# Optimization experiments

Measured on AMD Instinct MI355X. Metric: run time of the kernel, lower is better.

## Reference

```python
import jax, jax.numpy as jnp
import numpy as np

N_NODES = 50000
N_EDGES = 500000
IN_CH = 128
OUT_CH = 64
HEADS = 4


def setup_inputs() -> dict:
    key = jax.random.key(0)
    ks = jax.random.split(key, 9)
    x = jax.random.normal(ks[0], (N_NODES, IN_CH), dtype=jnp.float32)
    edge_index = jax.random.randint(ks[1], (2, N_EDGES), 0, N_NODES, dtype=jnp.int64)
    edge_weights = jax.random.uniform(ks[2], (N_EDGES, 1), dtype=jnp.float32)
    # xavier-uniform params, stored as [in, out] so y = x @ W
    def xavier(k, shape):
        fan_in, fan_out = shape
        lim = float(np.sqrt(6.0 / (fan_in + fan_out)))
        return jax.random.uniform(k, shape, minval=-lim, maxval=lim, dtype=jnp.float32)
    Wq = xavier(ks[3], (IN_CH, OUT_CH * HEADS))
    Wk = xavier(ks[4], (IN_CH, OUT_CH * HEADS))
    Wv = xavier(ks[5], (IN_CH, OUT_CH * HEADS))
    We = xavier(ks[6], (1, HEADS))
    Wout = xavier(ks[7], (OUT_CH * HEADS, OUT_CH))
    b_out = jnp.zeros((OUT_CH,), dtype=jnp.float32)
    return {"x": x, "edge_index": edge_index, "edge_weights": edge_weights,
            "Wq": Wq, "Wk": Wk, "Wv": Wv, "We": We, "Wout": Wout, "b_out": b_out}


def reference(x, edge_index, edge_weights, Wq, Wk, Wv, We, Wout, b_out):
    num_nodes = x.shape[0]
    src = edge_index[0]
    tgt = edge_index[1]
    x_src = x[src]                                    # [E, in]
    x_tgt = x[tgt]                                    # [E, in]
    q = (x_tgt @ Wq).reshape(-1, HEADS, OUT_CH)       # [E, H, C]
    k = (x_src @ Wk).reshape(-1, HEADS, OUT_CH)
    v = (x_src @ Wv).reshape(-1, HEADS, OUT_CH)
    attn = jnp.sum(q * k, axis=-1) / jnp.sqrt(jnp.float32(OUT_CH))  # [E, H]
    attn = attn + edge_weights @ We                   # [E, H]
    attn = jax.nn.leaky_relu(attn, negative_slope=0.2)
    attn = jax.nn.softmax(attn, axis=0)               # global softmax over edges (as in source)
    weighted_v = attn[..., None] * v                  # [E, H, C]
    out = jax.ops.segment_sum(weighted_v, tgt, num_segments=num_nodes)  # [N, H, C]
    out = out.reshape(num_nodes, HEADS * OUT_CH) @ Wout + b_out         # [N, out]
    if x.shape == out.shape:
        out = out + x
    return out
```

## Files before the change

kernel.cpp:

```cpp
#include <hip/hip_runtime.h>
#include <hip/hip_bf16.h>
#include <hip/hip_fp16.h>

#define N_NODES 50000
#define N_EDGES 500000
#define IN_CH   128
#define D       256
#define UDIM    512
#define OUT_CH  64
#define HEADS   4
#define NC      49
#define PCAP    1024

#define NB_X16  6250
#define NB_HIST 1954
#define NB_MB   256
#define NB_ZB   128
#define NB_GEMM 1564
#define NB_SCAT 1954

typedef _Float16 half8 __attribute__((ext_vector_type(8)));
typedef _Float16 half2_t __attribute__((ext_vector_type(2)));
typedef float   floatx4 __attribute__((ext_vector_type(4)));

__global__ __launch_bounds__(256) void k1_prep_kernel(const float* __restrict__ x,
                                                      __half* __restrict__ x16,
                                                      const int* __restrict__ ei,
                                                      int* __restrict__ cnt,
                                                      double* __restrict__ S,
                                                      const float* __restrict__ Wq,
                                                      const float* __restrict__ Wk,
                                                      const float* __restrict__ Wv,
                                                      const float* __restrict__ Wout,
                                                      __half* __restrict__ M16t,
                                                      __half* __restrict__ Zc16t) {
    __shared__ float sbuf[4][64];
    const int b = blockIdx.x, tid = threadIdx.x;
    if (b < NB_X16) {
        int i = b * 256 + tid;
        if (i < HEADS) S[i] = 0.0;
        int k = i * 4;
        if (k < N_NODES * IN_CH) {
            float4 v = *(const float4*)(x + k);
            union { __half2 h[2]; uint2 u; } pk;
            pk.h[0] = __floats2half2_rn(v.x, v.y);
            pk.h[1] = __floats2half2_rn(v.z, v.w);
            *(uint2*)(x16 + k) = pk.u;
        }
    } else if (b < NB_X16 + NB_HIST) {
        int e = (b - NB_X16) * 256 + tid;
        if (e < N_EDGES) atomicAdd(&cnt[ei[N_EDGES + e]], 1);
    } else if (b < NB_X16 + NB_HIST + NB_MB) {
        const int r = (b - NB_X16 - NB_HIST) * 2 + (tid >> 7);
        const int i = tid & 127;
        const int h = r >> 7, j = r & 127;
        float* buf = sbuf[tid >> 7];
        if (i < 64) buf[i] = Wk[(size_t)j * D + h * 64 + i];
        __syncthreads();
        const float4* qr = (const float4*)(Wq + (size_t)i * D + h * 64);
        float s = 0.f;
        #pragma unroll
        for (int c4 = 0; c4 < 16; ++c4) {
            float4 q = qr[c4];
            s += q.x * buf[c4 * 4] + q.y * buf[c4 * 4 + 1]
               + q.z * buf[c4 * 4 + 2] + q.w * buf[c4 * 4 + 3];
        }
        M16t[(size_t)r * IN_CH + i] = __float2half(s);
    } else {
        const int r = (b - NB_X16 - NB_HIST - NB_MB) * 4 + (tid >> 6);
        const int c = tid & 63;
        const int h = r >> 7, i = r & 127;
        float* buf = sbuf[tid >> 6];
        buf[c] = Wv[(size_t)i * D + h * 64 + c];
        __syncthreads();
        float s = 0.f;
        #pragma unroll 8
        for (int j = 0; j < 64; ++j)
            s += buf[j] * Wout[(size_t)(h * 64 + j) * OUT_CH + c];
        Zc16t[(size_t)c * UDIM + r] = __float2half(s);
    }
}

__global__ __launch_bounds__(256) void k2_scan_reduce_kernel(const int* __restrict__ cnt,
                                                             int* __restrict__ csum) {
    const int b = blockIdx.x, tid = threadIdx.x;
    const int lane = tid & 63, wid = tid >> 6;
    int s = 0;
    int idx0 = b * 1024 + tid * 4;
    #pragma unroll
    for (int i = 0; i < 4; ++i) {
        int idx = idx0 + i;
        if (idx < N_NODES) s += cnt[idx];
    }
    #pragma unroll
    for (int m = 1; m < 64; m <<= 1) s += __shfl_xor(s, m, 64);
    __shared__ int w4[4];
    if (lane == 0) w4[wid] = s;
    __syncthreads();
    if (tid == 0) csum[b] = w4[0] + w4[1] + w4[2] + w4[3];
}

__global__ __launch_bounds__(256) void k3_scan_chunks_kernel(int* __restrict__ cnt,
                                                             const int* __restrict__ csum,
                                                             int* __restrict__ rp) {
    __shared__ int stop[64];
    __shared__ int wsum[4];
    const int b = blockIdx.x, tid = threadIdx.x;
    const int lane = tid & 63, wid = tid >> 6;
    if (tid < 64) stop[tid] = (tid < NC) ? csum[tid] : 0;
    __syncthreads();
    int base = 0;
    for (int w = 0; w < b; ++w) base += stop[w];
    int v[4];
    const int idx0 = b * 1024 + tid * 4;
    #pragma unroll
    for (int i = 0; i < 4; ++i) {
        int idx = idx0 + i;
        v[i] = (idx < N_NODES) ? cnt[idx] : 0;
    }
    int tsum = v[0] + v[1] + v[2] + v[3];
    int x = tsum;
    #pragma unroll
    for (int d = 1; d < 64; d <<= 1) {
        int y = __shfl_up(x, d, 64);
        if (lane >= d) x += y;
    }
    if (lane == 63) wsum[wid] = x;
    __syncthreads();
    int woff = 0;
    for (int w = 0; w < wid; ++w) woff += wsum[w];
    int excl = base + woff + x - tsum;
    #pragma unroll
    for (int i = 0; i < 4; ++i) {
        int idx = idx0 + i;
        if (idx < N_NODES) { rp[idx] = excl; cnt[idx] = excl; }
        excl += v[i];
    }
}

__global__ __launch_bounds__(256) void k4_gemmu_scatter_kernel(const __half* __restrict__ x16,
                                                               const __half* __restrict__ M16t,
                                                               __half* __restrict__ u16,
                                                               const int* __restrict__ ei,
                                                               const float* __restrict__ ew,
                                                               int* __restrict__ cnt,
                                                               int2* __restrict__ payload) {
    __shared__ __half Ax[128][136];
    __shared__ __half Bm[128][136];
    const int tid = threadIdx.x;
    if (blockIdx.x >= NB_GEMM) {
        int e = (blockIdx.x - NB_GEMM) * 256 + tid;
        if (e < N_EDGES) {
            int s = ei[e], t = ei[N_EDGES + e];
            int pos = atomicAdd(&cnt[t], 1);
            payload[pos] = make_int2(s, __float_as_int(ew[e]));
        }
        return;
    }
    const int m0 = (blockIdx.x % 391) * 128;
    const int colbase = (blockIdx.x / 391) * 128;
    {
        const int r = tid >> 1, part = tid & 1;
        uint4 va[8];
        if (m0 + r < N_NODES) {
            const uint4* src = (const uint4*)(x16 + (size_t)(m0 + r) * IN_CH + part * 64);
            #pragma unroll
            for (int q = 0; q < 8; ++q) va[q] = src[q];
        } else {
            #pragma unroll
            for (int q = 0; q < 8; ++q) va[q] = make_uint4(0u, 0u, 0u, 0u);
        }
        uint4* da = (uint4*)&Ax[r][part * 64];
        #pragma unroll
        for (int q = 0; q < 8; ++q) da[q] = va[q];
        const uint4* sb = (const uint4*)(M16t + (size_t)(colbase + r) * IN_CH + part * 64);
        uint4* db = (uint4*)&Bm[r][part * 64];
        #pragma unroll
        for (int q = 0; q < 8; ++q) db[q] = sb[q];
    }
    __syncthreads();

    const int w = tid >> 6, lane = tid & 63;
    const int mrow = lane & 15, quad = lane >> 4;

    half8 a[2][4];
    #pragma unroll
    for (int mt = 0; mt < 2; ++mt)
        #pragma unroll
        for (int ks = 0; ks < 4; ++ks)
            a[mt][ks] = *(const half8*)&Ax[w * 32 + mt * 16 + mrow][ks * 32 + quad * 8];

    floatx4 acc[2][8];
    #pragma unroll
    for (int mt = 0; mt < 2; ++mt)
        #pragma unroll
        for (int nt = 0; nt < 8; ++nt)
            acc[mt][nt] = (floatx4){0.f, 0.f, 0.f, 0.f};

    #pragma unroll
    for (int nt = 0; nt < 8; ++nt) {
        #pragma unroll
        for (int ks = 0; ks < 4; ++ks) {
            half8 bfr = *(const half8*)&Bm[nt * 16 + mrow][ks * 32 + quad * 8];
            acc[0][nt] = __builtin_amdgcn_mfma_f32_16x16x32_f16(a[0][ks], bfr, acc[0][nt], 0, 0, 0);
            acc[1][nt] = __builtin_amdgcn_mfma_f32_16x16x32_f16(a[1][ks], bfr, acc[1][nt], 0, 0, 0);
        }
    }
    __syncthreads();
    #pragma unroll
    for (int mt = 0; mt < 2; ++mt)
        #pragma unroll
        for (int nt = 0; nt < 8; ++nt)
            #pragma unroll
            for (int r = 0; r < 4; ++r)
                Ax[w * 32 + mt * 16 + quad * 4 + r][nt * 16 + mrow] = __float2half(acc[mt][nt][r]);
    __syncthreads();
    {
        const int r = tid >> 1, part = tid & 1;
        if (m0 + r < N_NODES) {
            const uint4* s4 = (const uint4*)&Ax[r][part * 64];
            uint4* d4 = (uint4*)(u16 + (size_t)(m0 + r) * UDIM + colbase + part * 64);
            #pragma unroll
            for (int q = 0; q < 8; ++q) d4[q] = s4[q];
        }
    }
}

__global__ __launch_bounds__(256) void edge_fused_kernel(const __half* __restrict__ u16,
                                                         const __half* __restrict__ x16,
                                                         const int* __restrict__ rp,
                                                         const int* __restrict__ cnt,
                                                         const int2* __restrict__ payload,
                                                         const float* __restrict__ We,
                                                         __half* __restrict__ y16,
                                                         double* __restrict__ S) {
    __shared__ int2 pbuf[PCAP];
    __shared__ float sblk[4];
    const int tid = threadIdx.x;
    const int nodebase = blockIdx.x * 16;

    const int span0 = rp[nodebase];
    const int span1 = cnt[nodebase + 15];
    const int span_len = min(span1 - span0, PCAP);
    for (int i = tid; i < span_len; i += 256) pbuf[i] = payload[span0 + i];
    if (tid < 4) sblk[tid] = 0.f;
    __syncthreads();

    const int l16 = tid & 15;
    const int h = l16 >> 2;
    const int q = l16 & 3;
    const int node = nodebase + (tid >> 4);
    const float wev = We[h];

    uint4 ur4[4];
    {
        const uint4* ub = (const uint4*)(u16 + (size_t)node * UDIM + h * 128 + q * 32);
        ur4[0] = ub[0]; ur4[1] = ub[1]; ur4[2] = ub[2]; ur4[3] = ub[3];
    }
    const half2_t* uh = (const half2_t*)ur4;

    half2_t yacc[16];
    #pragma unroll
    for (int t = 0; t < 16; ++t) yacc[t] = (half2_t){(_Float16)0.f, (_Float16)0.f};

    float sacc = 0.f;
    const int start = rp[node];
    const int end = cnt[node];

    auto getpl = [&](int e) -> int2 {
        int idx = e - span0;
        return (idx < PCAP) ? pbuf[idx] : payload[e];
    };

    int2 pl = make_int2(0, 0);
    uint4 xr[4];
    if (start < end) {
        pl = getpl(start);
        const uint4* xb = (const uint4*)(x16 + (size_t)pl.x * IN_CH + q * 32);
        xr[0] = xb[0]; xr[1] = xb[1]; xr[2] = xb[2]; xr[3] = xb[3];
    }
    for (int e = start; e < end; ++e) {
        int2 pln = pl;
        uint4 xrn[4] = {xr[0], xr[1], xr[2], xr[3]};
        if (e + 1 < end) {
            pln = getpl(e + 1);
            const uint4* xb = (const uint4*)(x16 + (size_t)pln.x * IN_CH + q * 32);
            xrn[0] = xb[0]; xrn[1] = xb[1]; xrn[2] = xb[2]; xrn[3] = xb[3];
        }
        const half2_t* xh = (const half2_t*)xr;
        float dot = 0.f;
        #pragma unroll
        for (int t = 0; t < 16; ++t)
            dot = __builtin_amdgcn_fdot2(uh[t], xh[t], dot, false);
        dot += __shfl_xor(dot, 1, 16);
        dot += __shfl_xor(dot, 2, 16);
        float l = dot * 0.125f + __int_as_float(pl.y) * wev;
        l = fmaxf(l, 0.2f * l);
        float p = __expf(l);
        if (q == 0) sacc += p;
        half2_t p2 = (half2_t){(_Float16)p, (_Float16)p};
        #pragma unroll
        for (int t = 0; t < 16; ++t)
            yacc[t] = p2 * xh[t] + yacc[t];
        pl = pln;
        xr[0] = xrn[0]; xr[1] = xrn[1]; xr[2] = xrn[2]; xr[3] = xrn[3];
    }
    {
        uint4* yo = (uint4*)(y16 + (size_t)node * UDIM + h * 128 + q * 32);
        const uint4* ys = (const uint4*)yacc;
        yo[0] = ys[0]; yo[1] = ys[1]; yo[2] = ys[2]; yo[3] = ys[3];
    }
    __syncthreads();
    if (q == 0) atomicAdd(&sblk[h], sacc);
    __syncthreads();
    if (tid < 4) atomicAdd(&S[tid], (double)sblk[tid]);
}

__global__ __launch_bounds__(256) void gemm_out_mfma_kernel(const __half* __restrict__ y16,
                                                            const __half* __restrict__ Zc16t,
                                                            const double* __restrict__ S,
                                                            const float* __restrict__ b_out,
                                                            float* __restrict__ out) {
    __shared__ __half Ay[128][136];
    __shared__ __half Bz[64][136];
    __shared__ float invs_s[4];
    const int m0 = blockIdx.x * 128;
    const int tid = threadIdx.x;
    if (tid < 4) invs_s[tid] = (float)(1.0 / S[tid]);

    const int w = tid >> 6, lane = tid & 63;
    const int mrow = lane & 15, quad = lane >> 4;

    floatx4 result[2][4];
    #pragma unroll
    for (int mt = 0; mt < 2; ++mt)
        #pragma unroll
        for (int nt = 0; nt < 4; ++nt)
            result[mt][nt] = (floatx4){0.f, 0.f, 0.f, 0.f};

    for (int h = 0; h < HEADS; ++h) {
        {
            const int r = tid >> 1, part = tid & 1;
            uint4 va[8];
            if (m0 + r < N_NODES) {
                const uint4* src = (const uint4*)(y16 + (size_t)(m0 + r) * UDIM + h * 128 + part * 64);
                #pragma unroll
                for (int qq = 0; qq < 8; ++qq) va[qq] = src[qq];
            } else {
                #pragma unroll
                for (int qq = 0; qq < 8; ++qq) va[qq] = make_uint4(0u, 0u, 0u, 0u);
            }
            uint4* da = (uint4*)&Ay[r][part * 64];
            #pragma unroll
            for (int qq = 0; qq < 8; ++qq) da[qq] = va[qq];
        }
        {
            const int r = tid >> 2, part = tid & 3;
            const uint4* sb = (const uint4*)(Zc16t + (size_t)r * UDIM + h * 128 + part * 32);
            uint4* db = (uint4*)&Bz[r][part * 32];
            #pragma unroll
            for (int qq = 0; qq < 4; ++qq) db[qq] = sb[qq];
        }
        __syncthreads();

        half8 a[2][4];
        #pragma unroll
        for (int mt = 0; mt < 2; ++mt)
            #pragma unroll
            for (int ks = 0; ks < 4; ++ks)
                a[mt][ks] = *(const half8*)&Ay[w * 32 + mt * 16 + mrow][ks * 32 + quad * 8];

        floatx4 acc[2][4];
        #pragma unroll
        for (int mt = 0; mt < 2; ++mt)
            #pragma unroll
            for (int nt = 0; nt < 4; ++nt)
                acc[mt][nt] = (floatx4){0.f, 0.f, 0.f, 0.f};

        #pragma unroll
        for (int nt = 0; nt < 4; ++nt) {
            #pragma unroll
            for (int ks = 0; ks < 4; ++ks) {
                half8 bfr = *(const half8*)&Bz[nt * 16 + mrow][ks * 32 + quad * 8];
                acc[0][nt] = __builtin_amdgcn_mfma_f32_16x16x32_f16(a[0][ks], bfr, acc[0][nt], 0, 0, 0);
                acc[1][nt] = __builtin_amdgcn_mfma_f32_16x16x32_f16(a[1][ks], bfr, acc[1][nt], 0, 0, 0);
            }
        }
        const float inv = invs_s[h];
        #pragma unroll
        for (int mt = 0; mt < 2; ++mt)
            #pragma unroll
            for (int nt = 0; nt < 4; ++nt) {
                result[mt][nt][0] += inv * acc[mt][nt][0];
                result[mt][nt][1] += inv * acc[mt][nt][1];
                result[mt][nt][2] += inv * acc[mt][nt][2];
                result[mt][nt][3] += inv * acc[mt][nt][3];
            }
        __syncthreads();
    }
    float bcol[4];
    #pragma unroll
    for (int nt = 0; nt < 4; ++nt) bcol[nt] = b_out[nt * 16 + mrow];
    #pragma unroll
    for (int mt = 0; mt < 2; ++mt) {
        #pragma unroll
        for (int r = 0; r < 4; ++r) {
            int row = m0 + w * 32 + mt * 16 + quad * 4 + r;
            if (row < N_NODES) {
                float* dst = out + (size_t)row * OUT_CH;
                #pragma unroll
                for (int nt = 0; nt < 4; ++nt)
                    dst[nt * 16 + mrow] = result[mt][nt][r] + bcol[nt];
            }
        }
    }
}

extern "C" void kernel_launch(void* const* d_in, const int* in_sizes, int n_in,
                              void* d_out, int out_size, void* d_ws, size_t ws_size,
                              hipStream_t stream) {
    const float* x     = (const float*)d_in[0];
    const int*   ei    = (const int*)d_in[1];
    const float* ew    = (const float*)d_in[2];
    const float* Wq    = (const float*)d_in[3];
    const float* Wk    = (const float*)d_in[4];
    const float* Wv    = (const float*)d_in[5];
    const float* We    = (const float*)d_in[6];
    const float* Wout  = (const float*)d_in[7];
    const float* b_out = (const float*)d_in[8];
    float* out = (float*)d_out;

    __half* u16   = (__half*)d_ws;
    __half* y16   = u16 + (size_t)N_NODES * UDIM;
    __half* x16   = y16 + (size_t)N_NODES * UDIM;
    double* S     = (double*)(x16 + (size_t)N_NODES * IN_CH);
    __half* M16t  = (__half*)(S + HEADS);
    __half* Zc16t = M16t + UDIM * IN_CH;
    int*    rp    = (int*)(Zc16t + OUT_CH * UDIM);
    int*    cnt   = rp + N_NODES;
    int*    csum  = cnt + N_NODES;
    int2*   payload = (int2*)(csum + 64);

    hipMemsetAsync(cnt, 0, N_NODES * sizeof(int), stream);
    k1_prep_kernel<<<NB_X16 + NB_HIST + NB_MB + NB_ZB, 256, 0, stream>>>(
        x, x16, ei, cnt, S, Wq, Wk, Wv, Wout, M16t, Zc16t);
    k2_scan_reduce_kernel<<<NC, 256, 0, stream>>>(cnt, csum);
    k3_scan_chunks_kernel<<<NC, 256, 0, stream>>>(cnt, csum, rp);
    k4_gemmu_scatter_kernel<<<NB_GEMM + NB_SCAT, 256, 0, stream>>>(
        x16, M16t, u16, ei, ew, cnt, payload);
    edge_fused_kernel<<<N_NODES / 16, 256, 0, stream>>>(u16, x16, rp, cnt, payload, We, y16, S);
    gemm_out_mfma_kernel<<<(N_NODES + 127) / 128, 256, 0, stream>>>(y16, Zc16t, S, b_out, out);
}
```

Before: 270.5 us.

## Split GEMM/scatter kernel, drop LDS staging, double-buffer edge loop, use DPP reductions

The fused GEMM+scatter kernel is split into two separate launches. The u-projection GEMM now loads MFMA operands straight from global memory instead of staging them through LDS. The output GEMM is reworked the same way, with 64-row blocks and no shared memory. In the edge kernel, the per-edge loop gains a two-deep prefetch, splits the dot product into four independent accumulators, and replaces shfl_xor with DPP moves. These changes aim to cut LDS traffic, barriers and latency stalls, at the cost of redundant global/L2 loads and one extra kernel launch.

Result: slower. 310.8 us (+14.9%).

```diff
diff --git a/kernel.cpp b/kernel.cpp
--- a/kernel.cpp
+++ b/kernel.cpp
@@ -18,10 +18,18 @@
 #define NB_ZB   128
 #define NB_GEMM 1564
 #define NB_SCAT 1954
+#define NB_OUT  782
 
 typedef _Float16 half8 __attribute__((ext_vector_type(8)));
 typedef _Float16 half2_t __attribute__((ext_vector_type(2)));
 typedef float   floatx4 __attribute__((ext_vector_type(4)));
+
+__device__ __forceinline__ float dpp_xor1(float x) {
+    return __int_as_float(__builtin_amdgcn_mov_dpp(__float_as_int(x), 0xB1, 0xf, 0xf, true));
+}
+__device__ __forceinline__ float dpp_xor2(float x) {
+    return __int_as_float(__builtin_amdgcn_mov_dpp(__float_as_int(x), 0x4E, 0xf, 0xf, true));
+}
 
 __global__ __launch_bounds__(256) void k1_prep_kernel(const float* __restrict__ x,
                                                       __half* __restrict__ x16,
@@ -138,57 +146,25 @@
     }
 }
 
-__global__ __launch_bounds__(256) void k4_gemmu_scatter_kernel(const __half* __restrict__ x16,
-                                                               const __half* __restrict__ M16t,
-                                                               __half* __restrict__ u16,
-                                                               const int* __restrict__ ei,
-                                                               const float* __restrict__ ew,
-                                                               int* __restrict__ cnt,
-                                                               int2* __restrict__ payload) {
-    __shared__ __half Ax[128][136];
-    __shared__ __half Bm[128][136];
+__global__ __launch_bounds__(256) void k4a_gemm_kernel(const __half* __restrict__ x16,
+                                                       const __half* __restrict__ M16t,
+                                                       __half* __restrict__ u16) {
+    __shared__ __half Cst[128][136];
     const int tid = threadIdx.x;
-    if (blockIdx.x >= NB_GEMM) {
-        int e = (blockIdx.x - NB_GEMM) * 256 + tid;
-        if (e < N_EDGES) {
-            int s = ei[e], t = ei[N_EDGES + e];
-            int pos = atomicAdd(&cnt[t], 1);
-            payload[pos] = make_int2(s, __float_as_int(ew[e]));
-        }
-        return;
-    }
     const int m0 = (blockIdx.x % 391) * 128;
     const int colbase = (blockIdx.x / 391) * 128;
-    {
-        const int r = tid >> 1, part = tid & 1;
-        uint4 va[8];
-        if (m0 + r < N_NODES) {
-            const uint4* src = (const uint4*)(x16 + (size_t)(m0 + r) * IN_CH + part * 64);
-            #pragma unroll
-            for (int q = 0; q < 8; ++q) va[q] = src[q];
-        } else {
-            #pragma unroll
-            for (int q = 0; q < 8; ++q) va[q] = make_uint4(0u, 0u, 0u, 0u);
-        }
-        uint4* da = (uint4*)&Ax[r][part * 64];
-        #pragma unroll
-        for (int q = 0; q < 8; ++q) da[q] = va[q];
-        const uint4* sb = (const uint4*)(M16t + (size_t)(colbase + r) * IN_CH + part * 64);
-        uint4* db = (uint4*)&Bm[r][part * 64];
-        #pragma unroll
-        for (int q = 0; q < 8; ++q) db[q] = sb[q];
-    }
-    __syncthreads();
-
     const int w = tid >> 6, lane = tid & 63;
     const int mrow = lane & 15, quad = lane >> 4;
 
     half8 a[2][4];
     #pragma unroll
-    for (int mt = 0; mt < 2; ++mt)
-        #pragma unroll
-        for (int ks = 0; ks < 4; ++ks)
-            a[mt][ks] = *(const half8*)&Ax[w * 32 + mt * 16 + mrow][ks * 32 + quad * 8];
+    for (int mt = 0; mt < 2; ++mt) {
+        int row = m0 + w * 32 + mt * 16 + mrow;
+        row = min(row, N_NODES - 1);
+        const __half* ab = x16 + (size_t)row * IN_CH + quad * 8;
+        #pragma unroll
+        for (int ks = 0; ks < 4; ++ks) a[mt][ks] = *(const half8*)(ab + ks * 32);
+    }
 
     floatx4 acc[2][8];
     #pragma unroll
@@ -199,30 +175,43 @@
 
     #pragma unroll
     for (int nt = 0; nt < 8; ++nt) {
+        const __half* bb = M16t + (size_t)(colbase + nt * 16 + mrow) * IN_CH + quad * 8;
         #pragma unroll
         for (int ks = 0; ks < 4; ++ks) {
-            half8 bfr = *(const half8*)&Bm[nt * 16 + mrow][ks * 32 + quad * 8];
+            half8 bfr = *(const half8*)(bb + ks * 32);
             acc[0][nt] = __builtin_amdgcn_mfma_f32_16x16x32_f16(a[0][ks], bfr, acc[0][nt], 0, 0, 0);
             acc[1][nt] = __builtin_amdgcn_mfma_f32_16x16x32_f16(a[1][ks], bfr, acc[1][nt], 0, 0, 0);
         }
     }
-    __syncthreads();
+
     #pragma unroll
     for (int mt = 0; mt < 2; ++mt)
         #pragma unroll
         for (int nt = 0; nt < 8; ++nt)
             #pragma unroll
             for (int r = 0; r < 4; ++r)
-                Ax[w * 32 + mt * 16 + quad * 4 + r][nt * 16 + mrow] = __float2half(acc[mt][nt][r]);
+                Cst[w * 32 + mt * 16 + quad * 4 + r][nt * 16 + mrow] = __float2half(acc[mt][nt][r]);
     __syncthreads();
     {
         const int r = tid >> 1, part = tid & 1;
         if (m0 + r < N_NODES) {
-            const uint4* s4 = (const uint4*)&Ax[r][part * 64];
+            const uint4* s4 = (const uint4*)&Cst[r][part * 64];
             uint4* d4 = (uint4*)(u16 + (size_t)(m0 + r) * UDIM + colbase + part * 64);
             #pragma unroll
-            for (int q = 0; q < 8; ++q) d4[q] = s4[q];
-        }
+            for (int qq = 0; qq < 8; ++qq) d4[qq] = s4[qq];
+        }
+    }
+}
+
+__global__ __launch_bounds__(256) void k4b_scatter_kernel(const int* __restrict__ ei,
+                                                          const float* __restrict__ ew,
+                                                          int* __restrict__ cnt,
+                                                          int2* __restrict__ payload) {
+    int e = blockIdx.x * 256 + threadIdx.x;
+    if (e < N_EDGES) {
+        int s = ei[e], t = ei[N_EDGES + e];
+        int pos = atomicAdd(&cnt[t], 1);
+        payload[pos] = make_int2(s, __float_as_int(ew[e]));
     }
 }
 
@@ -271,40 +260,49 @@
         int idx = e - span0;
         return (idx < PCAP) ? pbuf[idx] : payload[e];
     };
-
-    int2 pl = make_int2(0, 0);
-    uint4 xr[4];
-    if (start < end) {
-        pl = getpl(start);
+    auto prefx = [&](const int2& pl, uint4* xr) {
         const uint4* xb = (const uint4*)(x16 + (size_t)pl.x * IN_CH + q * 32);
         xr[0] = xb[0]; xr[1] = xb[1]; xr[2] = xb[2]; xr[3] = xb[3];
-    }
-    for (int e = start; e < end; ++e) {
-        int2 pln = pl;
-        uint4 xrn[4] = {xr[0], xr[1], xr[2], xr[3]};
-        if (e + 1 < end) {
-            pln = getpl(e + 1);
-            const uint4* xb = (const uint4*)(x16 + (size_t)pln.x * IN_CH + q * 32);
-            xrn[0] = xb[0]; xrn[1] = xb[1]; xrn[2] = xb[2]; xrn[3] = xb[3];
-        }
+    };
+    auto process = [&](const int2& pl, const uint4* xr) {
         const half2_t* xh = (const half2_t*)xr;
-        float dot = 0.f;
-        #pragma unroll
-        for (int t = 0; t < 16; ++t)
-            dot = __builtin_amdgcn_fdot2(uh[t], xh[t], dot, false);
-        dot += __shfl_xor(dot, 1, 16);
-        dot += __shfl_xor(dot, 2, 16);
+        float d0 = 0.f, d1 = 0.f, d2 = 0.f, d3 = 0.f;
+        #pragma unroll
+        for (int t = 0; t < 4; ++t) {
+            d0 = __builtin_amdgcn_fdot2(uh[t],      xh[t],      d0, false);
+            d1 = __builtin_amdgcn_fdot2(uh[t + 4],  xh[t + 4],  d1, false);
+            d2 = __builtin_amdgcn_fdot2(uh[t + 8],  xh[t + 8],  d2, false);
+            d3 = __builtin_amdgcn_fdot2(uh[t + 12], xh[t + 12], d3, false);
+        }
+        float dot = (d0 + d1) + (d2 + d3);
+        dot += dpp_xor1(dot);
+        dot += dpp_xor2(dot);
         float l = dot * 0.125f + __int_as_float(pl.y) * wev;
         l = fmaxf(l, 0.2f * l);
         float p = __expf(l);
-        if (q == 0) sacc += p;
+        sacc += (q == 0) ? p : 0.f;
         half2_t p2 = (half2_t){(_Float16)p, (_Float16)p};
         #pragma unroll
         for (int t = 0; t < 16; ++t)
             yacc[t] = p2 * xh[t] + yacc[t];
-        pl = pln;
-        xr[0] = xrn[0]; xr[1] = xrn[1]; xr[2] = xrn[2]; xr[3] = xrn[3];
-    }
+    };
+
+    int2 plA = make_int2(0, 0), plB = make_int2(0, 0);
+    uint4 xrA[4], xrB[4];
+    if (start < end)     { plA = getpl(start);     prefx(plA, xrA); }
+    if (start + 1 < end) { plB = getpl(start + 1); prefx(plB, xrB); }
+
+    int e = start;
+    while (e < end) {
+        process(plA, xrA);
+        if (e + 2 < end) { plA = getpl(e + 2); prefx(plA, xrA); }
+        ++e;
+        if (e >= end) break;
+        process(plB, xrB);
+        if (e + 2 < end) { plB = getpl(e + 2); prefx(plB, xrB); }
+        ++e;
+    }
+
     {
         uint4* yo = (uint4*)(y16 + (size_t)node * UDIM + h * 128 + q * 32);
         const uint4* ys = (const uint4*)yacc;
@@ -321,97 +319,54 @@
                                                             const double* __restrict__ S,
                                                             const float* __restrict__ b_out,
                                                             float* __restrict__ out) {
-    __shared__ __half Ay[128][136];
-    __shared__ __half Bz[64][136];
-    __shared__ float invs_s[4];
-    const int m0 = blockIdx.x * 128;
     const int tid = threadIdx.x;
-    if (tid < 4) invs_s[tid] = (float)(1.0 / S[tid]);
-
     const int w = tid >> 6, lane = tid & 63;
     const int mrow = lane & 15, quad = lane >> 4;
-
-    floatx4 result[2][4];
-    #pragma unroll
-    for (int mt = 0; mt < 2; ++mt)
-        #pragma unroll
-        for (int nt = 0; nt < 4; ++nt)
-            result[mt][nt] = (floatx4){0.f, 0.f, 0.f, 0.f};
+    const int row0 = blockIdx.x * 64 + w * 16;
+
+    float invs[4];
+    #pragma unroll
+    for (int hh = 0; hh < HEADS; ++hh) invs[hh] = (float)(1.0 / S[hh]);
+
+    floatx4 result[4];
+    #pragma unroll
+    for (int nt = 0; nt < 4; ++nt) result[nt] = (floatx4){0.f, 0.f, 0.f, 0.f};
 
     for (int h = 0; h < HEADS; ++h) {
+        half8 a[4];
         {
-            const int r = tid >> 1, part = tid & 1;
-            uint4 va[8];
-            if (m0 + r < N_NODES) {
-                const uint4* src = (const uint4*)(y16 + (size_t)(m0 + r) * UDIM + h * 128 + part * 64);
-                #pragma unroll
-                for (int qq = 0; qq < 8; ++qq) va[qq] = src[qq];
-            } else {
-                #pragma unroll
-                for (int qq = 0; qq < 8; ++qq) va[qq] = make_uint4(0u, 0u, 0u, 0u);
+            int arow = min(row0 + mrow, N_NODES - 1);
+            const __half* ab = y16 + (size_t)arow * UDIM + h * 128 + quad * 8;
+            #pragma unroll
+            for (int ks = 0; ks < 4; ++ks) a[ks] = *(const half8*)(ab + ks * 32);
+        }
+        const float inv = invs[h];
+        #pragma unroll
+        for (int nt = 0; nt < 4; ++nt) {
+            floatx4 acc = (floatx4){0.f, 0.f, 0.f, 0.f};
+            const __half* bb = Zc16t + (size_t)(nt * 16 + mrow) * UDIM + h * 128 + quad * 8;
+            #pragma unroll
+            for (int ks = 0; ks < 4; ++ks) {
+                half8 bfr = *(const half8*)(bb + ks * 32);
+                acc = __builtin_amdgcn_mfma_f32_16x16x32_f16(a[ks], bfr, acc, 0, 0, 0);
             }
-            uint4* da = (uint4*)&Ay[r][part * 64];
-            #pragma unroll
-            for (int qq = 0; qq < 8; ++qq) da[qq] = va[qq];
-        }
-        {
-            const int r = tid >> 2, part = tid & 3;
-            const uint4* sb = (const uint4*)(Zc16t + (size_t)r * UDIM + h * 128 + part * 32);
-            uint4* db = (uint4*)&Bz[r][part * 32];
-            #pragma unroll
-            for (int qq = 0; qq < 4; ++qq) db[qq] = sb[qq];
-        }
-        __syncthreads();
-
-        half8 a[2][4];
-        #pragma unroll
-        for (int mt = 0; mt < 2; ++mt)
-            #pragma unroll
-            for (int ks = 0; ks < 4; ++ks)
-                a[mt][ks] = *(const half8*)&Ay[w * 32 + mt * 16 + mrow][ks * 32 + quad * 8];
-
-        floatx4 acc[2][4];
-        #pragma unroll
-        for (int mt = 0; mt < 2; ++mt)
+            result[nt][0] += inv * acc[0];
+            result[nt][1] += inv * acc[1];
+            result[nt][2] += inv * acc[2];
+            result[nt][3] += inv * acc[3];
+        }
+    }
+    float bcol[4];
+    #pragma unroll
+    for (int nt = 0; nt < 4; ++nt) bcol[nt] = b_out[nt * 16 + mrow];
+    #pragma unroll
+    for (int r = 0; r < 4; ++r) {
+        int row = row0 + quad * 4 + r;
+        if (row < N_NODES) {
+            float* dst = out + (size_t)row * OUT_CH;
             #pragma unroll
             for (int nt = 0; nt < 4; ++nt)
-                acc[mt][nt] = (floatx4){0.f, 0.f, 0.f, 0.f};
-
-        #pragma unroll
-        for (int nt = 0; nt < 4; ++nt) {
-            #pragma unroll
-            for (int ks = 0; ks < 4; ++ks) {
-                half8 bfr = *(const half8*)&Bz[nt * 16 + mrow][ks * 32 + quad * 8];
-                acc[0][nt] = __builtin_amdgcn_mfma_f32_16x16x32_f16(a[0][ks], bfr, acc[0][nt], 0, 0, 0);
-                acc[1][nt] = __builtin_amdgcn_mfma_f32_16x16x32_f16(a[1][ks], bfr, acc[1][nt], 0, 0, 0);
-            }
-        }
-        const float inv = invs_s[h];
-        #pragma unroll
-        for (int mt = 0; mt < 2; ++mt)
-            #pragma unroll
-            for (int nt = 0; nt < 4; ++nt) {
-                result[mt][nt][0] += inv * acc[mt][nt][0];
-                result[mt][nt][1] += inv * acc[mt][nt][1];
-                result[mt][nt][2] += inv * acc[mt][nt][2];
-                result[mt][nt][3] += inv * acc[mt][nt][3];
-            }
-        __syncthreads();
-    }
-    float bcol[4];
-    #pragma unroll
-    for (int nt = 0; nt < 4; ++nt) bcol[nt] = b_out[nt * 16 + mrow];
-    #pragma unroll
-    for (int mt = 0; mt < 2; ++mt) {
-        #pragma unroll
-        for (int r = 0; r < 4; ++r) {
-            int row = m0 + w * 32 + mt * 16 + quad * 4 + r;
-            if (row < N_NODES) {
-                float* dst = out + (size_t)row * OUT_CH;
-                #pragma unroll
-                for (int nt = 0; nt < 4; ++nt)
-                    dst[nt * 16 + mrow] = result[mt][nt][r] + bcol[nt];
-            }
+                dst[nt * 16 + mrow] = result[nt][r] + bcol[nt];
         }
     }
 }
@@ -446,8 +401,8 @@
         x, x16, ei, cnt, S, Wq, Wk, Wv, Wout, M16t, Zc16t);
     k2_scan_reduce_kernel<<<NC, 256, 0, stream>>>(cnt, csum);
     k3_scan_chunks_kernel<<<NC, 256, 0, stream>>>(cnt, csum, rp);
-    k4_gemmu_scatter_kernel<<<NB_GEMM + NB_SCAT, 256, 0, stream>>>(
-        x16, M16t, u16, ei, ew, cnt, payload);
+    k4a_gemm_kernel<<<NB_GEMM, 256, 0, stream>>>(x16, M16t, u16);
+    k4b_scatter_kernel<<<NB_SCAT, 256, 0, stream>>>(ei, ew, cnt, payload);
     edge_fused_kernel<<<N_NODES / 16, 256, 0, stream>>>(u16, x16, rp, cnt, payload, We, y16, S);
-    gemm_out_mfma_kernel<<<(N_NODES + 127) / 128, 256, 0, stream>>>(y16, Zc16t, S, b_out, out);
-}
+    gemm_out_mfma_kernel<<<NB_OUT, 256, 0, stream>>>(y16, Zc16t, S, b_out, out);
+}
```
